# Kernel tuning notes

Measured on AMD Instinct MI355X. Metric: run time of the kernel, lower is better.

## Reference

```python
import jax, jax.numpy as jnp
import numpy as np

B, N, C = 2, 20000, 128
E = 320000
H, COUT = 4, 64
HD = 256  # hidden_dim == H*COUT -> projection is None
ED = 16
L = 3  # LSTM layers


def setup_inputs() -> dict:
    key = jax.random.key(0)
    ks = jax.random.split(key, 16)
    return {
        "x": jax.random.normal(ks[0], (B, N, C), jnp.float32),
        "edge_index": jax.random.randint(ks[1], (2, E), 0, N),
        "edge_attr": jax.random.normal(ks[2], (E, ED), jnp.float32),
        "lin_w": jax.random.normal(ks[3], (C, H * COUT), jnp.float32) / np.sqrt(C),
        "att_src": jax.random.normal(ks[4], (1, H, COUT), jnp.float32) * 0.1,
        "att_dst": jax.random.normal(ks[5], (1, H, COUT), jnp.float32) * 0.1,
        "lin_edge_w": jax.random.normal(ks[6], (ED, H * COUT), jnp.float32) / np.sqrt(ED),
        "att_edge": jax.random.normal(ks[7], (1, H, COUT), jnp.float32) * 0.1,
        "gat_bias": jnp.zeros((H * COUT,), jnp.float32),
        "w_ih": jax.random.normal(ks[8], (L, 4 * HD, HD), jnp.float32) / np.sqrt(HD),
        "w_hh": jax.random.normal(ks[9], (L, 4 * HD, HD), jnp.float32) / np.sqrt(HD),
        "b_ih": jnp.zeros((L, 4 * HD), jnp.float32),
        "b_hh": jnp.zeros((L, 4 * HD), jnp.float32),
        "ln_g": jnp.ones((HD,), jnp.float32),
        "ln_b": jnp.zeros((HD,), jnp.float32),
    }


def reference(x, edge_index, edge_attr, lin_w, att_src, att_dst, lin_edge_w,
              att_edge, gat_bias, w_ih, w_hh, b_ih, b_hh, ln_g, ln_b):
    Bn = B * N
    # ---- GAT: linear transform ----
    xt = (x.reshape(Bn, C) @ lin_w).reshape(Bn, H, COUT)
    # batch-offset edge index, then append self-loops for every node
    off = (jnp.arange(B, dtype=edge_index.dtype) * N)[:, None]
    src = (edge_index[0][None, :] + off).reshape(-1)
    dst = (edge_index[1][None, :] + off).reshape(-1)
    loop = jnp.arange(Bn, dtype=edge_index.dtype)
    src = jnp.concatenate([src, loop])  # [Etot] = [B*E + B*N]
    dst = jnp.concatenate([dst, loop])
    # edge features: shared 2D edge_attr is repeated per batch, zeros on self-loops
    ea = (edge_attr @ lin_edge_w).reshape(E, H, COUT)
    ea = jnp.concatenate([jnp.tile(ea, (B, 1, 1)),
                          jnp.zeros((Bn, H, COUT), xt.dtype)], axis=0)
    # ---- message: gather, score, segment-softmax ----
    x_j = xt[src]  # [Etot, H, COUT]
    x_i = xt[dst]
    alpha = ((x_j * att_src).sum(-1) + (x_i * att_dst).sum(-1)
             + (ea * att_edge).sum(-1))  # [Etot, H]
    alpha = jax.nn.leaky_relu(alpha, 0.2)
    m = jax.ops.segment_max(alpha, dst, num_segments=Bn)
    alpha = jnp.exp(alpha - m[dst])
    s = jax.ops.segment_sum(alpha, dst, num_segments=Bn)
    alpha = alpha / (s[dst] + 1e-16)  # PyG softmax eps; dropout inactive (eval)
    # ---- aggregate (scatter-add) ----
    out = jax.ops.segment_sum(x_j * alpha[..., None], dst, num_segments=Bn)
    spatial = out.reshape(Bn, H * COUT) + gat_bias  # concat heads, [Bn, HD]
    # ---- 3-layer LSTM, seq_len=1, zero initial state (h_prev=None) ----
    h_in = spatial
    hs, cs = [], []
    for l in range(L):
        # h0 = c0 = 0 -> w_hh contributes nothing; inter-layer dropout inactive
        gates = h_in @ w_ih[l].T + b_ih[l] + b_hh[l]
        i, f, g, o = jnp.split(gates, 4, axis=-1)  # PyTorch gate order i,f,g,o
        c = jax.nn.sigmoid(i) * jnp.tanh(g)
        h = jax.nn.sigmoid(o) * jnp.tanh(c)
        hs.append(h)
        cs.append(c)
        h_in = h
    # ---- LayerNorm ----
    h_out = h_in.reshape(B, N, HD)
    mu = h_out.mean(-1, keepdims=True)
    var = ((h_out - mu) ** 2).mean(-1, keepdims=True)
    h_out = (h_out - mu) / jnp.sqrt(var + 1e-5) * ln_g + ln_b
    return h_out, jnp.stack(hs), jnp.stack(cs)
```

## Files before the change

kernel.cpp:

```cpp
#include <hip/hip_runtime.h>
#include <stdint.h>

#define NB_    20000
#define CB_    128
#define EE_    320000
#define BN_    40000
#define BE_    640000
#define ETOT_  680000

typedef __attribute__((ext_vector_type(4))) float f4;
typedef __attribute__((ext_vector_type(4))) unsigned short us4;
typedef __attribute__((ext_vector_type(4))) unsigned int ui4;
typedef __attribute__((ext_vector_type(8))) __bf16 bf16x8;

static __device__ __forceinline__ unsigned short f2bf(float f){
    union { float f; unsigned int u; } v; v.f = f;
    unsigned int u = v.u;
    u += 0x7FFFu + ((u >> 16) & 1u);
    return (unsigned short)(u >> 16);
}
static __device__ __forceinline__ float bf2f(unsigned short b){
    union { unsigned int u; float f; } v; v.u = ((unsigned int)b) << 16;
    return v.f;
}
static __device__ __forceinline__ float sigf(float x){ return 1.f/(1.f+__expf(-x)); }
static __device__ __forceinline__ float tanhfast(float x){ return 2.f/(1.f+__expf(-2.f*x)) - 1.f; }
static __device__ __forceinline__ f4 fmax4(f4 a, f4 b){
    f4 r; r[0]=fmaxf(a[0],b[0]); r[1]=fmaxf(a[1],b[1]); r[2]=fmaxf(a[2],b[2]); r[3]=fmaxf(a[3],b[3]); return r;
}

__global__ void w2_kernel(const float* __restrict__ lew, const float* __restrict__ ae,
                          float* __restrict__ W2){
    int t = threadIdx.x;
    int d = t >> 2, h = t & 3;
    float s = 0.f;
    for (int c = 0; c < 64; ++c) s += lew[d*256 + h*64 + c] * ae[h*64 + c];
    W2[d*4 + h] = s;
}

__global__ void pack_linwT_kernel(const float* __restrict__ lw, unsigned short* __restrict__ wt){
    int tid = blockIdx.x*256 + threadIdx.x;
    int n = tid >> 7, k = tid & 127;
    wt[n*128 + k] = f2bf(lw[k*256 + n]);
}

__global__ void pack_lstmw_kernel(const float* __restrict__ w_ih, unsigned short* __restrict__ Bp){
    int tid = blockIdx.x*256 + threadIdx.x;
    int l   = tid / 196608;
    int rem = tid - l*196608;
    int p = rem >> 8, k = rem & 255;
    int jb = p / 192, q2 = p - jb*192;
    int chunk = q2 / 48, r = q2 - chunk*48;
    int gate = r >> 4, jj = r & 15;
    int gor = (gate == 0) ? 0 : (gate == 1 ? 2 : 3);
    int srcrow = gor*256 + jb*64 + chunk*16 + jj;
    Bp[tid] = f2bf(w_ih[(l*1024 + srcrow)*256 + k]);
}

__global__ void pack_bias_kernel(const float* __restrict__ b_ih, const float* __restrict__ b_hh,
                                 float* __restrict__ bp){
    int tid = blockIdx.x*256 + threadIdx.x;
    if (tid >= 2304) return;
    int l = tid / 768, p = tid - l*768;
    int jb = p / 192, q2 = p - jb*192;
    int chunk = q2 / 48, r = q2 - chunk*48;
    int gate = r >> 4, jj = r & 15;
    int gor = (gate == 0) ? 0 : (gate == 1 ? 2 : 3);
    int srcrow = gor*256 + jb*64 + chunk*16 + jj;
    bp[tid] = b_ih[l*1024 + srcrow] + b_hh[l*1024 + srcrow];
}

__global__ __launch_bounds__(256) void gemm1_kernel(const float* __restrict__ x,
        const unsigned short* __restrict__ wt, unsigned short* __restrict__ xt){
    __shared__ unsigned short As[64*72];
    __shared__ unsigned short Bs[64*72];
    const int tid = threadIdx.x;
    const int bm = blockIdx.x, bn = blockIdx.y;
    const int lane = tid & 63, w = tid >> 6;
    const int wm = w & 1, wn = w >> 1;
    const int nl = lane & 15, q = lane >> 4;
    f4 acc[2][2] = {};
    for (int kc = 0; kc < 128; kc += 64) {
        #pragma unroll
        for (int it = 0; it < 4; ++it) {
            int s = tid + it*256;
            int row = s >> 4, c4 = s & 15;
            f4 v = *(const f4*)&x[(bm*64+row)*128 + kc + c4*4];
            us4 o; o[0]=f2bf(v[0]); o[1]=f2bf(v[1]); o[2]=f2bf(v[2]); o[3]=f2bf(v[3]);
            *(us4*)&As[row*72 + c4*4] = o;
        }
        #pragma unroll
        for (int it = 0; it < 2; ++it) {
            int s = tid + it*256;
            int row = s >> 3, c = s & 7;
            *(ui4*)&Bs[row*72 + c*8] = *(const ui4*)&wt[(bn*64+row)*128 + kc + c*8];
        }
        __syncthreads();
        #pragma unroll
        for (int kk = 0; kk < 64; kk += 32) {
            bf16x8 a[2], b[2];
            #pragma unroll
            for (int mt = 0; mt < 2; ++mt) a[mt] = *(const bf16x8*)&As[(wm*32 + mt*16 + nl)*72 + kk + q*8];
            #pragma unroll
            for (int nt = 0; nt < 2; ++nt) b[nt] = *(const bf16x8*)&Bs[(wn*32 + nt*16 + nl)*72 + kk + q*8];
            #pragma unroll
            for (int mt = 0; mt < 2; ++mt)
                #pragma unroll
                for (int nt = 0; nt < 2; ++nt)
                    acc[mt][nt] = __builtin_amdgcn_mfma_f32_16x16x32_bf16(a[mt], b[nt], acc[mt][nt], 0, 0, 0);
        }
        __syncthreads();
    }
    #pragma unroll
    for (int mt = 0; mt < 2; ++mt)
        #pragma unroll
        for (int nt = 0; nt < 2; ++nt)
            #pragma unroll
            for (int r = 0; r < 4; ++r) {
                int row = bm*64 + wm*32 + mt*16 + q*4 + r;
                int col = bn*64 + wn*32 + nt*16 + nl;
                xt[row*256 + col] = f2bf(acc[mt][nt][r]);
            }
}

__global__ __launch_bounds__(256) void scores_kernel(const unsigned short* __restrict__ xt,
        const float* __restrict__ att_src, const float* __restrict__ att_dst,
        float* __restrict__ s_src, float* __restrict__ s_dst){
    int n = blockIdx.x*4 + (threadIdx.x >> 6);
    int lane = threadIdx.x & 63;
    us4 xv = *(const us4*)&xt[n*256 + lane*4];
    f4 as = *(const f4*)&att_src[lane*4];
    f4 ad = *(const f4*)&att_dst[lane*4];
    float x0=bf2f(xv[0]), x1=bf2f(xv[1]), x2=bf2f(xv[2]), x3=bf2f(xv[3]);
    float ps = x0*as[0]+x1*as[1]+x2*as[2]+x3*as[3];
    float pd = x0*ad[0]+x1*ad[1]+x2*ad[2]+x3*ad[3];
    #pragma unroll
    for (int o = 1; o < 16; o <<= 1) { ps += __shfl_xor(ps, o, 64); pd += __shfl_xor(pd, o, 64); }
    if ((lane & 15) == 0) {
        s_src[n*4 + (lane>>4)] = ps;
        s_dst[n*4 + (lane>>4)] = pd;
    }
}

__global__ __launch_bounds__(256) void eascore_kernel(const float* __restrict__ ea,
        const float* __restrict__ W2, float* __restrict__ esc){
    __shared__ float w2s[64];
    if (threadIdx.x < 64) w2s[threadIdx.x] = W2[threadIdx.x];
    __syncthreads();
    int e = blockIdx.x*256 + threadIdx.x;
    if (e >= EE_) return;
    f4 acc = {};
    #pragma unroll
    for (int d = 0; d < 16; ++d) {
        float v = ea[e*16 + d];
        f4 wv = *(const f4*)&w2s[d*4];
        acc += v * wv;
    }
    *(f4*)&esc[e*4] = acc;
}

__global__ __launch_bounds__(256) void deghist_kernel(const int* __restrict__ ei, int* __restrict__ deg){
    int e = blockIdx.x*256 + threadIdx.x;
    if (e >= ETOT_) return;
    int dst;
    if (e < BE_) { int b = e / EE_, ee = e - b*EE_; dst = ei[EE_ + ee] + b*NB_; }
    else dst = e - BE_;
    atomicAdd(&deg[dst], 1);
}

__global__ __launch_bounds__(256) void scan1_kernel(const int* __restrict__ deg,
        int* __restrict__ inc, int* __restrict__ bsum){
    __shared__ int sd[256];
    int t = threadIdx.x, i = blockIdx.x*256 + t;
    int v = (i < BN_) ? deg[i] : 0;
    sd[t] = v; __syncthreads();
    #pragma unroll
    for (int d = 1; d < 256; d <<= 1) {
        int x = (t >= d) ? sd[t-d] : 0; __syncthreads();
        sd[t] += x; __syncthreads();
    }
    inc[i] = sd[t];
    if (t == 255) bsum[blockIdx.x] = sd[255];
}

__global__ __launch_bounds__(256) void scan2_kernel(const int* __restrict__ bsum,
        int* __restrict__ bpre, int nb){
    __shared__ int sd[256];
    int t = threadIdx.x;
    int v = (t < nb) ? bsum[t] : 0;
    sd[t] = v; __syncthreads();
    #pragma unroll
    for (int d = 1; d < 256; d <<= 1) {
        int x = (t >= d) ? sd[t-d] : 0; __syncthreads();
        sd[t] += x; __syncthreads();
    }
    if (t < nb) bpre[t] = sd[t] - v;
}

__global__ __launch_bounds__(256) void scan3_kernel(const int* __restrict__ inc,
        const int* __restrict__ deg, const int* __restrict__ bpre,
        int* __restrict__ offs, int* __restrict__ cur){
    int i = blockIdx.x*256 + threadIdx.x;
    if (i >= BN_) return;
    int o = inc[i] - deg[i] + bpre[blockIdx.x];
    offs[i] = o; cur[i] = o;
}

__global__ __launch_bounds__(256) void scatter_kernel(const int* __restrict__ ei,
        const float* __restrict__ s_src, const float* __restrict__ s_dst,
        const float* __restrict__ esc, int* __restrict__ cur,
        int* __restrict__ csr_src, float* __restrict__ csr_alpha){
    int e = blockIdx.x*256 + threadIdx.x;
    if (e >= ETOT_) return;
    int src, dst; f4 a;
    if (e < BE_) {
        int b = e / EE_, ee = e - b*EE_;
        src = ei[ee] + b*NB_;
        dst = ei[EE_ + ee] + b*NB_;
        a = *(const f4*)&esc[ee*4];
    } else {
        src = dst = e - BE_;
        a = (f4){0.f, 0.f, 0.f, 0.f};
    }
    a += *(const f4*)&s_src[src*4];
    a += *(const f4*)&s_dst[dst*4];
    #pragma unroll
    for (int h = 0; h < 4; ++h) a[h] = (a[h] > 0.f) ? a[h] : 0.2f*a[h];
    int pos = atomicAdd(&cur[dst], 1);
    csr_src[pos] = src;
    *(f4*)&csr_alpha[pos*4] = a;
}

__global__ __launch_bounds__(256) void aggregate_kernel(const int* __restrict__ offs,
        const int* __restrict__ deg, const int* __restrict__ csr_src,
        const float* __restrict__ csr_alpha, const unsigned short* __restrict__ xt,
        const float* __restrict__ gat_bias, unsigned short* __restrict__ spat){
    int n = blockIdx.x*4 + (threadIdx.x >> 6);
    int lane = threadIdx.x & 63;
    int start = offs[n], d = deg[n];
    f4 mv = {-1e30f, -1e30f, -1e30f, -1e30f};
    for (int i = lane; i < d; i += 64)
        mv = fmax4(mv, *(const f4*)&csr_alpha[(start+i)*4]);
    #pragma unroll
    for (int o = 1; o < 64; o <<= 1) {
        f4 t; t[0]=__shfl_xor(mv[0],o,64); t[1]=__shfl_xor(mv[1],o,64);
        t[2]=__shfl_xor(mv[2],o,64); t[3]=__shfl_xor(mv[3],o,64);
        mv = fmax4(mv, t);
    }
    f4 sv = {};
    for (int i = lane; i < d; i += 64) {
        f4 a = *(const f4*)&csr_alpha[(start+i)*4];
        sv[0] += __expf(a[0]-mv[0]); sv[1] += __expf(a[1]-mv[1]);
        sv[2] += __expf(a[2]-mv[2]); sv[3] += __expf(a[3]-mv[3]);
    }
    #pragma unroll
    for (int o = 1; o < 64; o <<= 1) {
        sv[0]+=__shfl_xor(sv[0],o,64); sv[1]+=__shfl_xor(sv[1],o,64);
        sv[2]+=__shfl_xor(sv[2],o,64); sv[3]+=__shfl_xor(sv[3],o,64);
    }
    int h = lane >> 4;
    float mh = (h==0)?mv[0]:(h==1)?mv[1]:(h==2)?mv[2]:mv[3];
    float sh = (h==0)?sv[0]:(h==1)?sv[1]:(h==2)?sv[2]:sv[3];
    f4 accv = {};
    for (int base = 0; base < d; base += 64) {
        int cnt = min(64, d - base);
        int srcl = (base + lane < d) ? csr_src[start+base+lane] : 0;
        for (int i = 0; i < cnt; ++i) {
            int srcn = __shfl(srcl, i, 64);
            float av = csr_alpha[(start+base+i)*4 + h];
            float ew = __expf(av - mh);
            us4 xv = *(const us4*)&xt[srcn*256 + lane*4];
            accv[0] += ew * bf2f(xv[0]);
            accv[1] += ew * bf2f(xv[1]);
            accv[2] += ew * bf2f(xv[2]);
            accv[3] += ew * bf2f(xv[3]);
        }
    }
    float invs = 1.f / (sh + 1e-16f);
    f4 gb = *(const f4*)&gat_bias[lane*4];
    accv = accv * invs + gb;
    us4 o4; o4[0]=f2bf(accv[0]); o4[1]=f2bf(accv[1]); o4[2]=f2bf(accv[2]); o4[3]=f2bf(accv[3]);
    *(us4*)&spat[n*256 + lane*4] = o4;
}

__global__ __launch_bounds__(256) void lstm_kernel(const unsigned short* __restrict__ A,
        const unsigned short* __restrict__ Bp, const float* __restrict__ bias,
        float* __restrict__ hs_out, float* __restrict__ cs_out, unsigned short* __restrict__ hnext){
    __shared__ unsigned short As[64*72];
    __shared__ unsigned short Bs[192*72];
    const int tid = threadIdx.x;
    const int bm = blockIdx.x, jb = blockIdx.y;
    const int lane = tid & 63, w = tid >> 6;
    const int nl = lane & 15, q = lane >> 4;
    f4 acc[4][3] = {};
    const unsigned short* Bbase = Bp + jb*192*256;
    for (int kc = 0; kc < 256; kc += 64) {
        #pragma unroll
        for (int it = 0; it < 2; ++it) {
            int s = tid + it*256;
            int row = s >> 3, c = s & 7;
            *(ui4*)&As[row*72 + c*8] = *(const ui4*)&A[(bm*64+row)*256 + kc + c*8];
        }
        #pragma unroll
        for (int it = 0; it < 6; ++it) {
            int s = tid + it*256;
            int row = s >> 3, c = s & 7;
            *(ui4*)&Bs[row*72 + c*8] = *(const ui4*)&Bbase[row*256 + kc + c*8];
        }
        __syncthreads();
        #pragma unroll
        for (int kk = 0; kk < 64; kk += 32) {
            bf16x8 a[4], b[3];
            #pragma unroll
            for (int mt = 0; mt < 4; ++mt) a[mt] = *(const bf16x8*)&As[(mt*16 + nl)*72 + kk + q*8];
            #pragma unroll
            for (int gt = 0; gt < 3; ++gt) b[gt] = *(const bf16x8*)&Bs[(w*48 + gt*16 + nl)*72 + kk + q*8];
            #pragma unroll
            for (int mt = 0; mt < 4; ++mt)
                #pragma unroll
                for (int gt = 0; gt < 3; ++gt)
                    acc[mt][gt] = __builtin_amdgcn_mfma_f32_16x16x32_bf16(a[mt], b[gt], acc[mt][gt], 0, 0, 0);
        }
        __syncthreads();
    }
    const int j = jb*64 + w*16 + nl;
    const float bi = bias[jb*192 + w*48 +  0 + nl];
    const float bg = bias[jb*192 + w*48 + 16 + nl];
    const float bo = bias[jb*192 + w*48 + 32 + nl];
    #pragma unroll
    for (int mt = 0; mt < 4; ++mt)
        #pragma unroll
        for (int r = 0; r < 4; ++r) {
            int m = bm*64 + mt*16 + q*4 + r;
            float iv = acc[mt][0][r] + bi;
            float gv = acc[mt][1][r] + bg;
            float ov = acc[mt][2][r] + bo;
            float c = sigf(iv) * tanhfast(gv);
            float hh = sigf(ov) * tanhfast(c);
            cs_out[m*256 + j] = c;
            hs_out[m*256 + j] = hh;
            if (hnext) hnext[m*256 + j] = f2bf(hh);
        }
}

__global__ __launch_bounds__(256) void ln_kernel(const float* __restrict__ hin,
        const float* __restrict__ g, const float* __restrict__ b, float* __restrict__ out){
    int n = blockIdx.x*4 + (threadIdx.x >> 6);
    int lane = threadIdx.x & 63;
    f4 v = *(const f4*)&hin[n*256 + lane*4];
    float s = v[0]+v[1]+v[2]+v[3];
    float ss = v[0]*v[0]+v[1]*v[1]+v[2]*v[2]+v[3]*v[3];
    #pragma unroll
    for (int o = 1; o < 64; o <<= 1) { s += __shfl_xor(s,o,64); ss += __shfl_xor(ss,o,64); }
    float mu = s * (1.f/256.f);
    float var = ss * (1.f/256.f) - mu*mu;
    float rstd = rsqrtf(var + 1e-5f);
    f4 gg = *(const f4*)&g[lane*4], bb = *(const f4*)&b[lane*4];
    f4 o4 = (v - mu) * rstd * gg + bb;
    *(f4*)&out[n*256 + lane*4] = o4;
}

static inline char* carve(char*& p, size_t bytes){
    char* r = p; p += (bytes + 255) & ~(size_t)255; return r;
}

extern "C" void kernel_launch(void* const* d_in, const int* in_sizes, int n_in,
                              void* d_out, int out_size, void* d_ws, size_t ws_size,
                              hipStream_t stream){
    const float* x         = (const float*)d_in[0];
    const int*   ei        = (const int*)  d_in[1];
    const float* edge_attr = (const float*)d_in[2];
    const float* lin_w     = (const float*)d_in[3];
    const float* att_src   = (const float*)d_in[4];
    const float* att_dst   = (const float*)d_in[5];
    const float* lin_edge_w= (const float*)d_in[6];
    const float* att_edge  = (const float*)d_in[7];
    const float* gat_bias  = (const float*)d_in[8];
    const float* w_ih      = (const float*)d_in[9];
    const float* b_ih      = (const float*)d_in[11];
    const float* b_hh      = (const float*)d_in[12];
    const float* ln_g      = (const float*)d_in[13];
    const float* ln_b      = (const float*)d_in[14];

    float* out = (float*)d_out;
    float* hs_base = out + 10240000;
    float* cs_base = out + 40960000;

    unsigned short* xt   = (unsigned short*)(out + 0);
    float* esc           = out + 10240000;
    int*   csr_src       = (int*)(out + 40960000);
    float* csr_alpha     = out + 41640000;
    unsigned short* spat = (unsigned short*)(out + 51200000);
    unsigned short* h0   = (unsigned short*)(out + 61440000);
    unsigned short* h1   = (unsigned short*)(out + 0);

    char* p = (char*)d_ws;
    float* W2          = (float*)carve(p, 64*4);
    float* s_src       = (float*)carve(p, (size_t)BN_*4*4);
    float* s_dst       = (float*)carve(p, (size_t)BN_*4*4);
    unsigned short* lwT= (unsigned short*)carve(p, 32768*2);
    unsigned short* Bp = (unsigned short*)carve(p, 589824*2);
    float* biasP       = (float*)carve(p, 2304*4);
    int* deg           = (int*)carve(p, BN_*4);
    int* inc           = (int*)carve(p, 157*256*4);
    int* bsum          = (int*)carve(p, 256*4);
    int* bpre          = (int*)carve(p, 256*4);
    int* offs          = (int*)carve(p, BN_*4);
    int* cur           = (int*)carve(p, BN_*4);

    hipMemsetAsync(deg, 0, BN_*4, stream);
    w2_kernel<<<1, 64, 0, stream>>>(lin_edge_w, att_edge, W2);
    pack_linwT_kernel<<<128, 256, 0, stream>>>(lin_w, lwT);
    pack_lstmw_kernel<<<2304, 256, 0, stream>>>(w_ih, Bp);
    pack_bias_kernel<<<9, 256, 0, stream>>>(b_ih, b_hh, biasP);

    gemm1_kernel<<<dim3(625, 4), 256, 0, stream>>>(x, lwT, xt);
    scores_kernel<<<10000, 256, 0, stream>>>(xt, att_src, att_dst, s_src, s_dst);
    eascore_kernel<<<1250, 256, 0, stream>>>(edge_attr, W2, esc);

    deghist_kernel<<<2657, 256, 0, stream>>>(ei, deg);
    scan1_kernel<<<157, 256, 0, stream>>>(deg, inc, bsum);
    scan2_kernel<<<1, 256, 0, stream>>>(bsum, bpre, 157);
    scan3_kernel<<<157, 256, 0, stream>>>(inc, deg, bpre, offs, cur);
    scatter_kernel<<<2657, 256, 0, stream>>>(ei, s_src, s_dst, esc, cur, csr_src, csr_alpha);
    aggregate_kernel<<<10000, 256, 0, stream>>>(offs, deg, csr_src, csr_alpha, xt, gat_bias, spat);

    lstm_kernel<<<dim3(625, 4), 256, 0, stream>>>(spat, Bp,          biasP,        hs_base,           cs_base,           h0);
    lstm_kernel<<<dim3(625, 4), 256, 0, stream>>>(h0,   Bp + 196608, biasP + 768,  hs_base + 10240000, cs_base + 10240000, h1);
    lstm_kernel<<<dim3(625, 4), 256, 0, stream>>>(h1,   Bp + 393216, biasP + 1536, hs_base + 20480000, cs_base + 20480000, (unsigned short*)nullptr);

    ln_kernel<<<10000, 256, 0, stream>>>(hs_base + 20480000, ln_g, ln_b, out);
}
```

Measured before the change: 604.3 us.

## Drop softmax max pass, unroll gather-aggregate, use direct-to-LDS swizzled loads in LSTM

The scatter kernel now computes exp of the leaky-relu score directly and accumulates per-destination sums with float atomics, so the aggregate kernel no longer needs the max and sum passes over the edge scores. The aggregate gather loop is unrolled by four to keep more independent loads in flight. The LSTM GEMM switches to global_load_lds transfers into an XOR-swizzled, unpadded shared layout to avoid the register round trip and bank conflicts. Skipping the max subtraction risks overflow for large scores, and the float atomics add contention and make summation order nondeterministic.

```diff
diff --git a/kernel.cpp b/kernel.cpp
--- a/kernel.cpp
+++ b/kernel.cpp
@@ -25,8 +25,9 @@
 }
 static __device__ __forceinline__ float sigf(float x){ return 1.f/(1.f+__expf(-x)); }
 static __device__ __forceinline__ float tanhfast(float x){ return 2.f/(1.f+__expf(-2.f*x)) - 1.f; }
-static __device__ __forceinline__ f4 fmax4(f4 a, f4 b){
-    f4 r; r[0]=fmaxf(a[0],b[0]); r[1]=fmaxf(a[1],b[1]); r[2]=fmaxf(a[2],b[2]); r[3]=fmaxf(a[3],b[3]); return r;
+static __device__ __forceinline__ void gl_lds16(const void* g, void* l){
+    __builtin_amdgcn_global_load_lds((const __attribute__((address_space(1))) void*)g,
+                                     (__attribute__((address_space(3))) void*)l, 16, 0, 0);
 }
 
 __global__ void w2_kernel(const float* __restrict__ lew, const float* __restrict__ ae,
@@ -209,7 +210,7 @@
 __global__ __launch_bounds__(256) void scatter_kernel(const int* __restrict__ ei,
         const float* __restrict__ s_src, const float* __restrict__ s_dst,
         const float* __restrict__ esc, int* __restrict__ cur,
-        int* __restrict__ csr_src, float* __restrict__ csr_alpha){
+        int* __restrict__ csr_src, float* __restrict__ csr_e, float* __restrict__ ssum){
     int e = blockIdx.x*256 + threadIdx.x;
     if (e >= ETOT_) return;
     int src, dst; f4 a;
@@ -224,56 +225,60 @@
     }
     a += *(const f4*)&s_src[src*4];
     a += *(const f4*)&s_dst[dst*4];
-    #pragma unroll
-    for (int h = 0; h < 4; ++h) a[h] = (a[h] > 0.f) ? a[h] : 0.2f*a[h];
+    f4 ev;
+    #pragma unroll
+    for (int h = 0; h < 4; ++h) {
+        float v = (a[h] > 0.f) ? a[h] : 0.2f*a[h];
+        ev[h] = __expf(v);
+    }
     int pos = atomicAdd(&cur[dst], 1);
     csr_src[pos] = src;
-    *(f4*)&csr_alpha[pos*4] = a;
+    *(f4*)&csr_e[pos*4] = ev;
+    atomicAdd(&ssum[dst*4 + 0], ev[0]);
+    atomicAdd(&ssum[dst*4 + 1], ev[1]);
+    atomicAdd(&ssum[dst*4 + 2], ev[2]);
+    atomicAdd(&ssum[dst*4 + 3], ev[3]);
 }
 
 __global__ __launch_bounds__(256) void aggregate_kernel(const int* __restrict__ offs,
         const int* __restrict__ deg, const int* __restrict__ csr_src,
-        const float* __restrict__ csr_alpha, const unsigned short* __restrict__ xt,
+        const float* __restrict__ csr_e, const float* __restrict__ ssum,
+        const unsigned short* __restrict__ xt,
         const float* __restrict__ gat_bias, unsigned short* __restrict__ spat){
     int n = blockIdx.x*4 + (threadIdx.x >> 6);
     int lane = threadIdx.x & 63;
     int start = offs[n], d = deg[n];
-    f4 mv = {-1e30f, -1e30f, -1e30f, -1e30f};
-    for (int i = lane; i < d; i += 64)
-        mv = fmax4(mv, *(const f4*)&csr_alpha[(start+i)*4]);
-    #pragma unroll
-    for (int o = 1; o < 64; o <<= 1) {
-        f4 t; t[0]=__shfl_xor(mv[0],o,64); t[1]=__shfl_xor(mv[1],o,64);
-        t[2]=__shfl_xor(mv[2],o,64); t[3]=__shfl_xor(mv[3],o,64);
-        mv = fmax4(mv, t);
-    }
-    f4 sv = {};
-    for (int i = lane; i < d; i += 64) {
-        f4 a = *(const f4*)&csr_alpha[(start+i)*4];
-        sv[0] += __expf(a[0]-mv[0]); sv[1] += __expf(a[1]-mv[1]);
-        sv[2] += __expf(a[2]-mv[2]); sv[3] += __expf(a[3]-mv[3]);
-    }
-    #pragma unroll
-    for (int o = 1; o < 64; o <<= 1) {
-        sv[0]+=__shfl_xor(sv[0],o,64); sv[1]+=__shfl_xor(sv[1],o,64);
-        sv[2]+=__shfl_xor(sv[2],o,64); sv[3]+=__shfl_xor(sv[3],o,64);
-    }
     int h = lane >> 4;
-    float mh = (h==0)?mv[0]:(h==1)?mv[1]:(h==2)?mv[2]:mv[3];
-    float sh = (h==0)?sv[0]:(h==1)?sv[1]:(h==2)?sv[2]:sv[3];
+    float sh = ssum[n*4 + h];
     f4 accv = {};
     for (int base = 0; base < d; base += 64) {
         int cnt = min(64, d - base);
-        int srcl = (base + lane < d) ? csr_src[start+base+lane] : 0;
-        for (int i = 0; i < cnt; ++i) {
-            int srcn = __shfl(srcl, i, 64);
-            float av = csr_alpha[(start+base+i)*4 + h];
-            float ew = __expf(av - mh);
-            us4 xv = *(const us4*)&xt[srcn*256 + lane*4];
-            accv[0] += ew * bf2f(xv[0]);
-            accv[1] += ew * bf2f(xv[1]);
-            accv[2] += ew * bf2f(xv[2]);
-            accv[3] += ew * bf2f(xv[3]);
+        int idx0 = start + base;
+        int srcl = (base + lane < d) ? csr_src[idx0 + lane] : 0;
+        int i = 0;
+        for (; i + 4 <= cnt; i += 4) {
+            int s0 = __shfl(srcl, i,   64);
+            int s1 = __shfl(srcl, i+1, 64);
+            int s2 = __shfl(srcl, i+2, 64);
+            int s3 = __shfl(srcl, i+3, 64);
+            float e0 = csr_e[(idx0+i  )*4 + h];
+            float e1 = csr_e[(idx0+i+1)*4 + h];
+            float e2 = csr_e[(idx0+i+2)*4 + h];
+            float e3 = csr_e[(idx0+i+3)*4 + h];
+            us4 x0 = *(const us4*)&xt[s0*256 + lane*4];
+            us4 x1 = *(const us4*)&xt[s1*256 + lane*4];
+            us4 x2 = *(const us4*)&xt[s2*256 + lane*4];
+            us4 x3 = *(const us4*)&xt[s3*256 + lane*4];
+            #pragma unroll
+            for (int c = 0; c < 4; ++c)
+                accv[c] += e0*bf2f(x0[c]) + e1*bf2f(x1[c]) + e2*bf2f(x2[c]) + e3*bf2f(x3[c]);
+        }
+        for (; i < cnt; ++i) {
+            int s0 = __shfl(srcl, i, 64);
+            float e0 = csr_e[(idx0+i)*4 + h];
+            us4 x0 = *(const us4*)&xt[s0*256 + lane*4];
+            #pragma unroll
+            for (int c = 0; c < 4; ++c) accv[c] += e0*bf2f(x0[c]);
         }
     }
     float invs = 1.f / (sh + 1e-16f);
@@ -286,35 +291,39 @@
 __global__ __launch_bounds__(256) void lstm_kernel(const unsigned short* __restrict__ A,
         const unsigned short* __restrict__ Bp, const float* __restrict__ bias,
         float* __restrict__ hs_out, float* __restrict__ cs_out, unsigned short* __restrict__ hnext){
-    __shared__ unsigned short As[64*72];
-    __shared__ unsigned short Bs[192*72];
+    __shared__ unsigned short As[64*64];
+    __shared__ unsigned short Bs[192*64];
     const int tid = threadIdx.x;
     const int bm = blockIdx.x, jb = blockIdx.y;
     const int lane = tid & 63, w = tid >> 6;
     const int nl = lane & 15, q = lane >> 4;
+    const int rsub = lane >> 3, csub = lane & 7;
+    const int swz = ((csub ^ rsub) << 4);
     f4 acc[4][3] = {};
-    const unsigned short* Bbase = Bp + jb*192*256;
+    const char* Ab = (const char*)A + ((size_t)(bm*64 + rsub))*512 + swz;
+    const char* Bb = (const char*)(Bp + (size_t)jb*192*256) + (size_t)rsub*512 + swz;
     for (int kc = 0; kc < 256; kc += 64) {
         #pragma unroll
-        for (int it = 0; it < 2; ++it) {
-            int s = tid + it*256;
-            int row = s >> 3, c = s & 7;
-            *(ui4*)&As[row*72 + c*8] = *(const ui4*)&A[(bm*64+row)*256 + kc + c*8];
-        }
-        #pragma unroll
-        for (int it = 0; it < 6; ++it) {
-            int s = tid + it*256;
-            int row = s >> 3, c = s & 7;
-            *(ui4*)&Bs[row*72 + c*8] = *(const ui4*)&Bbase[row*256 + kc + c*8];
+        for (int i = 0; i < 2; ++i) {
+            int t = 2*w + i;
+            gl_lds16(Ab + (size_t)t*4096 + kc*2, (char*)As + t*1024);
+        }
+        #pragma unroll
+        for (int i = 0; i < 6; ++i) {
+            int t = 6*w + i;
+            gl_lds16(Bb + (size_t)t*4096 + kc*2, (char*)Bs + t*1024);
         }
         __syncthreads();
         #pragma unroll
         for (int kk = 0; kk < 64; kk += 32) {
+            const int cswz = (kk*2 + q*16) ^ ((nl & 7) << 4);
             bf16x8 a[4], b[3];
             #pragma unroll
-            for (int mt = 0; mt < 4; ++mt) a[mt] = *(const bf16x8*)&As[(mt*16 + nl)*72 + kk + q*8];
-            #pragma unroll
-            for (int gt = 0; gt < 3; ++gt) b[gt] = *(const bf16x8*)&Bs[(w*48 + gt*16 + nl)*72 + kk + q*8];
+            for (int mt = 0; mt < 4; ++mt)
+                a[mt] = *(const bf16x8*)((const char*)As + (mt*16 + nl)*128 + cswz);
+            #pragma unroll
+            for (int gt = 0; gt < 3; ++gt)
+                b[gt] = *(const bf16x8*)((const char*)Bs + (w*48 + gt*16 + nl)*128 + cswz);
             #pragma unroll
             for (int mt = 0; mt < 4; ++mt)
                 #pragma unroll
@@ -387,9 +396,10 @@
     float* cs_base = out + 40960000;
 
     unsigned short* xt   = (unsigned short*)(out + 0);
+    float* ssum          = out + 5120000;
     float* esc           = out + 10240000;
     int*   csr_src       = (int*)(out + 40960000);
-    float* csr_alpha     = out + 41640000;
+    float* csr_e         = out + 41640000;
     unsigned short* spat = (unsigned short*)(out + 51200000);
     unsigned short* h0   = (unsigned short*)(out + 61440000);
     unsigned short* h1   = (unsigned short*)(out + 0);
@@ -409,6 +419,7 @@
     int* cur           = (int*)carve(p, BN_*4);
 
     hipMemsetAsync(deg, 0, BN_*4, stream);
+    hipMemsetAsync(ssum, 0, (size_t)BN_*4*4, stream);
     w2_kernel<<<1, 64, 0, stream>>>(lin_edge_w, att_edge, W2);
     pack_linwT_kernel<<<128, 256, 0, stream>>>(lin_w, lwT);
     pack_lstmw_kernel<<<2304, 256, 0, stream>>>(w_ih, Bp);
@@ -422,10 +433,10 @@
     scan1_kernel<<<157, 256, 0, stream>>>(deg, inc, bsum);
     scan2_kernel<<<1, 256, 0, stream>>>(bsum, bpre, 157);
     scan3_kernel<<<157, 256, 0, stream>>>(inc, deg, bpre, offs, cur);
-    scatter_kernel<<<2657, 256, 0, stream>>>(ei, s_src, s_dst, esc, cur, csr_src, csr_alpha);
-    aggregate_kernel<<<10000, 256, 0, stream>>>(offs, deg, csr_src, csr_alpha, xt, gat_bias, spat);
-
-    lstm_kernel<<<dim3(625, 4), 256, 0, stream>>>(spat, Bp,          biasP,        hs_base,           cs_base,           h0);
+    scatter_kernel<<<2657, 256, 0, stream>>>(ei, s_src, s_dst, esc, cur, csr_src, csr_e, ssum);
+    aggregate_kernel<<<10000, 256, 0, stream>>>(offs, deg, csr_src, csr_e, ssum, xt, gat_bias, spat);
+
+    lstm_kernel<<<dim3(625, 4), 256, 0, stream>>>(spat, Bp,          biasP,        hs_base,            cs_base,            h0);
     lstm_kernel<<<dim3(625, 4), 256, 0, stream>>>(h0,   Bp + 196608, biasP + 768,  hs_base + 10240000, cs_base + 10240000, h1);
     lstm_kernel<<<dim3(625, 4), 256, 0, stream>>>(h1,   Bp + 393216, biasP + 1536, hs_base + 20480000, cs_base + 20480000, (unsigned short*)nullptr);
 
```

New measurement: 721.7 us. 19.4% more time.
